# Optimization experiments

Measured on AMD Instinct MI355X. Metric: run time of the kernel, lower is better.

The kernel has to match this reference:

```python
import jax, jax.numpy as jnp
import numpy as np

H = 16         # num query heads
KV = 8         # num kv heads
HD = 64        # head_dim
WINDOW = 512   # sliding window size
ROPE_BASE = 10000.0


def rotate_half(x):
    x1, x2 = x[..., : x.shape[-1] // 2], x[..., x.shape[-1] // 2 :]
    return jnp.concatenate((-x2, x1), axis=-1)


def rope_cos_sin(seq_len, dim, dtype):
    inv_freq = 1.0 / (ROPE_BASE ** (jnp.arange(0, dim, 2, dtype=jnp.float32) / dim))
    t = jnp.arange(seq_len, dtype=jnp.float32)
    freqs = jnp.outer(t, inv_freq)              # [S, dim/2]
    emb = jnp.concatenate((freqs, freqs), axis=-1)  # [S, dim]
    return jnp.cos(emb).astype(dtype), jnp.sin(emb).astype(dtype)


def setup_inputs() -> dict:
    key = jax.random.key(0)
    ks = jax.random.split(key, 5)
    B, S, D = 2, 2048, 1024
    std = 0.02
    return {
        "hidden_states": jax.random.normal(ks[0], (B, S, D), dtype=jnp.float32),
        "Wq": jax.random.normal(ks[1], (D, H * HD), dtype=jnp.float32) * std,
        "Wk": jax.random.normal(ks[2], (D, KV * HD), dtype=jnp.float32) * std,
        "Wv": jax.random.normal(ks[3], (D, KV * HD), dtype=jnp.float32) * std,
        "Wo": jax.random.normal(ks[4], (H * HD, D), dtype=jnp.float32) * std,
    }


def reference(hidden_states, Wq, Wk, Wv, Wo):
    B, S, D = hidden_states.shape
    n_rep = H // KV

    q = (hidden_states @ Wq).reshape(B, S, H, HD).transpose(0, 2, 1, 3)   # [B,H,S,hd]
    k = (hidden_states @ Wk).reshape(B, S, KV, HD).transpose(0, 2, 1, 3)  # [B,KV,S,hd]
    v = (hidden_states @ Wv).reshape(B, S, KV, HD).transpose(0, 2, 1, 3)

    cos, sin = rope_cos_sin(S, HD, q.dtype)  # [S,hd]
    cos = cos[None, None]
    sin = sin[None, None]
    q = q * cos + rotate_half(q) * sin
    k = k * cos + rotate_half(k) * sin

    # repeat kv heads for GQA ([:, :, None] expand + reshape == repeat along head axis)
    k = jnp.repeat(k, n_rep, axis=1)  # [B,H,S,hd]
    v = jnp.repeat(v, n_rep, axis=1)

    scores = jnp.einsum("bhqd,bhkd->bhqk", q, k) / jnp.sqrt(jnp.asarray(HD, q.dtype))
    i = jnp.arange(S)[:, None]
    j = jnp.arange(S)[None, :]
    allowed = (j <= i) & (j >= i - WINDOW)  # causal + sliding window
    scores = jnp.where(allowed[None, None], scores, -jnp.inf)

    attn = jax.nn.softmax(scores, axis=-1)
    out = jnp.einsum("bhqk,bhkd->bhqd", attn, v)          # [B,H,S,hd]
    out = out.transpose(0, 2, 1, 3).reshape(B, S, H * HD)  # [B,S,D]
    return out @ Wo
```

## Files before the change

### kernel.cpp

```cpp
#include <hip/hip_runtime.h>
#include <hip/hip_bf16.h>

typedef __attribute__((ext_vector_type(8))) short short8;
typedef __attribute__((ext_vector_type(4))) float f32x4;

#define S_LEN 2048
#define NH 16
#define NKV 8
#define HD 64
#define WIN 512
#define DMODEL 1024
#define LOG2_10000 13.287712379549449f

#define GLOAD16(g, l)                                                        \
    __builtin_amdgcn_global_load_lds(                                        \
        (const __attribute__((address_space(1))) unsigned int*)(g),          \
        (__attribute__((address_space(3))) unsigned int*)(l), 16, 0, 0)

__global__ void cast_bf16_kernel(const float* __restrict__ X,
                                 __hip_bfloat16* __restrict__ Y, int n) {
    int i = (blockIdx.x * 256 + threadIdx.x) * 4;
    if (i + 3 < n) {
        float4 v = *reinterpret_cast<const float4*>(X + i);
        Y[i + 0] = __float2bfloat16(v.x);
        Y[i + 1] = __float2bfloat16(v.y);
        Y[i + 2] = __float2bfloat16(v.z);
        Y[i + 3] = __float2bfloat16(v.w);
    }
}

__global__ void transpose_cast4_kernel(const float* __restrict__ W0,
                                       const float* __restrict__ W1,
                                       const float* __restrict__ W2,
                                       const float* __restrict__ W3,
                                       __hip_bfloat16* __restrict__ WqkvT,
                                       __hip_bfloat16* __restrict__ WoT) {
    __shared__ float tile[32][33];
    const int K = DMODEL;
    const float* W;
    __hip_bfloat16* WT;
    int N;
    switch (blockIdx.z) {
        case 0: W = W0; WT = WqkvT;                          N = 1024; break;
        case 1: W = W1; WT = WqkvT + (size_t)1024 * K;       N = 512;  break;
        case 2: W = W2; WT = WqkvT + (size_t)1536 * K;       N = 512;  break;
        default: W = W3; WT = WoT;                           N = 1024; break;
    }
    if ((int)blockIdx.x * 32 >= N) return;
    int nx = blockIdx.x * 32 + threadIdx.x;
    int k0 = blockIdx.y * 32;
#pragma unroll
    for (int r = 0; r < 4; ++r) {
        int k = k0 + threadIdx.y + r * 8;
        tile[threadIdx.y + r * 8][threadIdx.x] = W[(size_t)k * N + nx];
    }
    __syncthreads();
#pragma unroll
    for (int r = 0; r < 4; ++r) {
        int nn = blockIdx.x * 32 + threadIdx.y + r * 8;
        int kk = k0 + threadIdx.x;
        WT[(size_t)nn * K + kk] = __float2bfloat16(tile[threadIdx.x][threadIdx.y + r * 8]);
    }
}

template <int MODE>
__global__ __launch_bounds__(128) void gemm128_kernel(
    const __hip_bfloat16* __restrict__ A,
    const __hip_bfloat16* __restrict__ BT,
    void* __restrict__ o0, void* __restrict__ o1, void* __restrict__ o2,
    int N, int K) {
    __shared__ __hip_bfloat16 ldsA[2][128 * 32];
    __shared__ __hip_bfloat16 ldsB[2][64 * 32];
    const int tx = threadIdx.x;
    const int wave = tx >> 6;
    const int lane = tx & 63;
    const int l16 = lane & 15;
    const int quad = lane >> 4;
    const int col0 = blockIdx.x * 64;
    const int row0 = blockIdx.y * 128;
    const int wrow = wave * 64;

    f32x4 acc[4][4] = {};

    const int arow = tx >> 2;
    const int kc8 = (tx & 3) * 8;
    const __hip_bfloat16* gA = A + (size_t)(row0 + arow) * K + kc8;
    const __hip_bfloat16* gB = BT + (size_t)(col0 + arow) * K + kc8;

    auto stage = [&](int k0, int bf) {
        char* lA = (char*)(&ldsA[bf][0]) + tx * 16;
        char* lB = (char*)(&ldsB[bf][0]) + tx * 16;
#pragma unroll
        for (int r = 0; r < 4; ++r)
            GLOAD16(gA + (size_t)(r * 32) * K + k0, lA + r * 2048);
#pragma unroll
        for (int r = 0; r < 2; ++r)
            GLOAD16(gB + (size_t)(r * 32) * K + k0, lB + r * 2048);
    };

    stage(0, 0);
    int buf = 0;
    for (int k0 = 0; k0 < K; k0 += 32) {
        __syncthreads();
        if (k0 + 32 < K) stage(k0 + 32, buf ^ 1);
        short8 af[4], bf4[4];
#pragma unroll
        for (int i = 0; i < 4; ++i) {
            af[i] = *reinterpret_cast<const short8*>(
                &ldsA[buf][0] + (wrow + i * 16 + l16) * 32 + quad * 8);
            bf4[i] = *reinterpret_cast<const short8*>(
                &ldsB[buf][0] + (i * 16 + l16) * 32 + quad * 8);
        }
#pragma unroll
        for (int mi = 0; mi < 4; ++mi)
#pragma unroll
            for (int ni = 0; ni < 4; ++ni)
                acc[mi][ni] = __builtin_amdgcn_mfma_f32_16x16x32_bf16(
                    af[mi], bf4[ni], acc[mi][ni], 0, 0, 0);
        buf ^= 1;
    }

    const int rbase = row0 + wrow;
    if (MODE == 0) {
        const int cbaseg = col0;
        const bool isQ = (cbaseg < DMODEL);
        const bool isK = (cbaseg >= DMODEL) && (cbaseg < DMODEL + 512);
        if (isQ || isK) {
            float invf[2];
            invf[0] = exp2f(-(float)(l16)      * (LOG2_10000 / 32.0f));
            invf[1] = exp2f(-(float)(16 + l16) * (LOG2_10000 / 32.0f));
#pragma unroll
            for (int mi = 0; mi < 4; ++mi)
#pragma unroll
                for (int r = 0; r < 4; ++r) {
                    int srow = (rbase + mi * 16 + quad * 4 + r) & (S_LEN - 1);
#pragma unroll
                    for (int ni = 0; ni < 2; ++ni) {
                        float ang = (float)srow * invf[ni];
                        float c = __cosf(ang), s = __sinf(ang);
                        float x1 = acc[mi][ni][r], x2 = acc[mi][ni + 2][r];
                        acc[mi][ni][r]     = x1 * c - x2 * s;
                        acc[mi][ni + 2][r] = x2 * c + x1 * s;
                    }
                }
            __hip_bfloat16* Co = (__hip_bfloat16*)(isQ ? o0 : o1);
            int cbase = isQ ? cbaseg : cbaseg - DMODEL;
            int rowstride = isQ ? (NH * HD) : (NKV * HD);
#pragma unroll
            for (int mi = 0; mi < 4; ++mi)
#pragma unroll
                for (int ni = 0; ni < 4; ++ni) {
                    size_t col = cbase + ni * 16 + l16;
#pragma unroll
                    for (int r = 0; r < 4; ++r)
                        Co[(size_t)(rbase + mi * 16 + quad * 4 + r) * rowstride + col] =
                            __float2bfloat16(acc[mi][ni][r]);
                }
        } else {
            __hip_bfloat16* VTo = (__hip_bfloat16*)o2;
            int bb = row0 >> 11;
#pragma unroll
            for (int mi = 0; mi < 4; ++mi) {
                int s = ((rbase + mi * 16 + quad * 4) & (S_LEN - 1));
#pragma unroll
                for (int ni = 0; ni < 4; ++ni) {
                    int colv = cbaseg - 1536 + ni * 16 + l16;
                    int vh = colv >> 6, d = colv & 63;
                    alignas(8) __hip_bfloat16 hv[4];
#pragma unroll
                    for (int r = 0; r < 4; ++r) hv[r] = __float2bfloat16(acc[mi][ni][r]);
                    *reinterpret_cast<ushort4*>(
                        VTo + ((size_t)(bb * NKV + vh) * HD + d) * S_LEN + s) =
                        *reinterpret_cast<ushort4*>(hv);
                }
            }
        }
    } else {
        float* Co = (float*)o0;
#pragma unroll
        for (int mi = 0; mi < 4; ++mi)
#pragma unroll
            for (int ni = 0; ni < 4; ++ni) {
                size_t col = col0 + ni * 16 + l16;
#pragma unroll
                for (int r = 0; r < 4; ++r)
                    Co[(size_t)(rbase + mi * 16 + quad * 4 + r) * N + col] = acc[mi][ni][r];
            }
    }
}

__global__ __launch_bounds__(256, 3) void attn_mfma_kernel(
    const __hip_bfloat16* __restrict__ Q,
    const __hip_bfloat16* __restrict__ K,
    const __hip_bfloat16* __restrict__ VT,
    __hip_bfloat16* __restrict__ O) {
    __shared__ __hip_bfloat16 ldsK[2][64][64];
    __shared__ __hip_bfloat16 ldsVT[2][64][64];
    __shared__ __hip_bfloat16 ldsP[4][2][16][80];
    const int tx = threadIdx.x;
    const int wave = tx >> 6;
    const int lane = tx & 63;
    const int l16 = lane & 15;
    const int quad = lane >> 4;
    const int q0 = blockIdx.x * 64;
    const int kvh = blockIdx.y;
    const int b = blockIdx.z;
    const int qi = q0 + wave * 16 + l16;

    short8 aq[2][2];
#pragma unroll
    for (int hh = 0; hh < 2; ++hh) {
        const __hip_bfloat16* qp =
            Q + (size_t)(b * S_LEN + qi) * (NH * HD) + (2 * kvh + hh) * HD + quad * 8;
        aq[hh][0] = *reinterpret_cast<const short8*>(qp);
        aq[hh][1] = *reinterpret_cast<const short8*>(qp + 32);
    }
    f32x4 acc_o[2][4] = {};
    float m[2] = {-1e30f, -1e30f}, l[2] = {0.f, 0.f};
    const float SL2 = 0.125f * 1.4426950408889634f;

    const int s_row = tx >> 3;
    const int s_c8 = (((tx & 7) ^ (s_row & 7))) * 8;
    const int sw = (l16 & 7);
    auto stage = [&](int j0, int bf) {
        char* lk = (char*)(&ldsK[bf][0][0]) + tx * 16;
        char* lv = (char*)(&ldsVT[bf][0][0]) + tx * 16;
#pragma unroll
        for (int r = 0; r < 2; ++r) {
            int row = s_row + r * 32;
            GLOAD16(K + (size_t)(b * S_LEN + j0 + row) * (NKV * HD) + kvh * HD + s_c8,
                    lk + r * 4096);
            GLOAD16(VT + ((size_t)(b * NKV + kvh) * HD + row) * S_LEN + j0 + s_c8,
                    lv + r * 4096);
        }
    };

    const int kstart = (q0 >= WIN) ? (q0 - WIN) : 0;
    stage(kstart, 0);
    int buf = 0;

    for (int j0 = kstart; j0 <= q0; j0 += 64) {
        __syncthreads();
        if (j0 + 64 <= q0) stage(j0 + 64, buf ^ 1);

        f32x4 sacc[2][4] = {};
#pragma unroll
        for (int t = 0; t < 4; ++t) {
            const __hip_bfloat16* krow = &ldsK[buf][t * 16 + l16][0];
            short8 bk0 = *reinterpret_cast<const short8*>(krow + ((quad ^ sw) * 8));
            short8 bk1 = *reinterpret_cast<const short8*>(krow + (((4 + quad) ^ sw) * 8));
            sacc[0][t] = __builtin_amdgcn_mfma_f32_16x16x32_bf16(bk0, aq[0][0], sacc[0][t], 0, 0, 0);
            sacc[0][t] = __builtin_amdgcn_mfma_f32_16x16x32_bf16(bk1, aq[0][1], sacc[0][t], 0, 0, 0);
            sacc[1][t] = __builtin_amdgcn_mfma_f32_16x16x32_bf16(bk0, aq[1][0], sacc[1][t], 0, 0, 0);
            sacc[1][t] = __builtin_amdgcn_mfma_f32_16x16x32_bf16(bk1, aq[1][1], sacc[1][t], 0, 0, 0);
        }

        const bool need_mask = (j0 == q0) || (q0 >= WIN && j0 == kstart);
#pragma unroll
        for (int hh = 0; hh < 2; ++hh) {
            float sv[4][4];
            if (need_mask) {
#pragma unroll
                for (int t = 0; t < 4; ++t)
#pragma unroll
                    for (int r = 0; r < 4; ++r) {
                        int j = j0 + t * 16 + quad * 4 + r;
                        bool ok = (j <= qi) && (j + WIN >= qi);
                        sv[t][r] = ok ? sacc[hh][t][r] * SL2 : -1e30f;
                    }
            } else {
#pragma unroll
                for (int t = 0; t < 4; ++t)
#pragma unroll
                    for (int r = 0; r < 4; ++r) sv[t][r] = sacc[hh][t][r] * SL2;
            }
            float cm = -1e30f;
#pragma unroll
            for (int t = 0; t < 4; ++t)
#pragma unroll
                for (int r = 0; r < 4; ++r) cm = fmaxf(cm, sv[t][r]);
            cm = fmaxf(cm, __shfl_xor(cm, 16));
            cm = fmaxf(cm, __shfl_xor(cm, 32));
            float mn = fmaxf(m[hh], cm);
            float alpha = exp2f(m[hh] - mn);
            m[hh] = mn;
            float sp = 0.f;
#pragma unroll
            for (int t = 0; t < 4; ++t)
#pragma unroll
                for (int r = 0; r < 4; ++r) { sv[t][r] = exp2f(sv[t][r] - mn); sp += sv[t][r]; }
            sp += __shfl_xor(sp, 16);
            sp += __shfl_xor(sp, 32);
            l[hh] = l[hh] * alpha + sp;
#pragma unroll
            for (int t = 0; t < 4; ++t)
#pragma unroll
                for (int r = 0; r < 4; ++r) acc_o[hh][t][r] *= alpha;
#pragma unroll
            for (int t = 0; t < 4; ++t) {
                alignas(8) __hip_bfloat16 hp[4];
#pragma unroll
                for (int r = 0; r < 4; ++r) hp[r] = __float2bfloat16(sv[t][r]);
                *reinterpret_cast<ushort4*>(&ldsP[wave][hh][l16][t * 16 + quad * 4]) =
                    *reinterpret_cast<ushort4*>(hp);
            }
        }

#pragma unroll
        for (int ks = 0; ks < 2; ++ks) {
            short8 pf0 = *reinterpret_cast<const short8*>(
                &ldsP[wave][0][l16][ks * 32 + quad * 8]);
            short8 pf1 = *reinterpret_cast<const short8*>(
                &ldsP[wave][1][l16][ks * 32 + quad * 8]);
#pragma unroll
            for (int t = 0; t < 4; ++t) {
                const __hip_bfloat16* vrow = &ldsVT[buf][t * 16 + l16][0];
                short8 vf = *reinterpret_cast<const short8*>(
                    vrow + (((ks * 4 + quad) ^ sw) * 8));
                acc_o[0][t] = __builtin_amdgcn_mfma_f32_16x16x32_bf16(vf, pf0, acc_o[0][t], 0, 0, 0);
                acc_o[1][t] = __builtin_amdgcn_mfma_f32_16x16x32_bf16(vf, pf1, acc_o[1][t], 0, 0, 0);
            }
        }
        buf ^= 1;
    }

#pragma unroll
    for (int hh = 0; hh < 2; ++hh) {
        float inv = 1.f / l[hh];
        __hip_bfloat16* op =
            O + (size_t)(b * S_LEN + qi) * (NH * HD) + (2 * kvh + hh) * HD;
#pragma unroll
        for (int t = 0; t < 4; ++t) {
            alignas(8) __hip_bfloat16 ho[4];
#pragma unroll
            for (int r = 0; r < 4; ++r) ho[r] = __float2bfloat16(acc_o[hh][t][r] * inv);
            *reinterpret_cast<ushort4*>(op + t * 16 + quad * 4) =
                *reinterpret_cast<ushort4*>(ho);
        }
    }
}

extern "C" void kernel_launch(void* const* d_in, const int* in_sizes, int n_in,
                              void* d_out, int out_size, void* d_ws, size_t ws_size,
                              hipStream_t stream) {
    const float* X  = (const float*)d_in[0];
    const float* Wq = (const float*)d_in[1];
    const float* Wk = (const float*)d_in[2];
    const float* Wv = (const float*)d_in[3];
    const float* Wo = (const float*)d_in[4];
    float* out = (float*)d_out;

    const int ROWS = 2 * S_LEN;
    char* ws = (char*)d_ws;
    size_t off = 0;
    __hip_bfloat16* Xb     = (__hip_bfloat16*)(ws + off); off += (size_t)ROWS * DMODEL * 2;
    __hip_bfloat16* WqkvT  = (__hip_bfloat16*)(ws + off); off += (size_t)2048 * DMODEL * 2;
    __hip_bfloat16* WoT    = (__hip_bfloat16*)(ws + off); off += (size_t)DMODEL * DMODEL * 2;
    __hip_bfloat16* Qb     = (__hip_bfloat16*)(ws + off); off += (size_t)ROWS * (NH * HD) * 2;
    __hip_bfloat16* Kb     = (__hip_bfloat16*)(ws + off); off += (size_t)ROWS * (NKV * HD) * 2;
    __hip_bfloat16* VTg    = (__hip_bfloat16*)(ws + off); off += (size_t)ROWS * (NKV * HD) * 2;
    __hip_bfloat16* Ob     = (__hip_bfloat16*)(ws + off); off += (size_t)ROWS * (NH * HD) * 2;

    cast_bf16_kernel<<<(ROWS * DMODEL) / (256 * 4), 256, 0, stream>>>(X, Xb, ROWS * DMODEL);
    transpose_cast4_kernel<<<dim3(32, 32, 4), dim3(32, 8), 0, stream>>>(
        Wq, Wk, Wv, Wo, WqkvT, WoT);

    gemm128_kernel<0><<<dim3(2048 / 64, ROWS / 128), 128, 0, stream>>>(
        Xb, WqkvT, Qb, Kb, VTg, 2048, DMODEL);

    attn_mfma_kernel<<<dim3(S_LEN / 64, NKV, 2), 256, 0, stream>>>(Qb, Kb, VTg, Ob);

    gemm128_kernel<1><<<dim3(DMODEL / 64, ROWS / 128), 128, 0, stream>>>(
        Ob, WoT, out, nullptr, nullptr, DMODEL, DMODEL);
}
```

Baseline: 166.4 us.

## Split attention grid per query head instead of per KV head pair

The attention kernel now launches one block per query head rather than one per KV head handling both grouped query heads. This doubles the grid to 1024 blocks and halves per-thread register state, and launch bounds are raised to 4 blocks per CU. The P tile in LDS shrinks to one head and uses an XOR-swizzled layout in place of padding to avoid bank conflicts. In exchange, each K/V tile is now loaded twice from global memory, once for each head sharing it.

```diff
diff --git a/kernel.cpp b/kernel.cpp
--- a/kernel.cpp
+++ b/kernel.cpp
@@ -189,34 +189,34 @@
     }
 }
 
-__global__ __launch_bounds__(256, 3) void attn_mfma_kernel(
+__global__ __launch_bounds__(256, 4) void attn_mfma_kernel(
     const __hip_bfloat16* __restrict__ Q,
     const __hip_bfloat16* __restrict__ K,
     const __hip_bfloat16* __restrict__ VT,
     __hip_bfloat16* __restrict__ O) {
     __shared__ __hip_bfloat16 ldsK[2][64][64];
     __shared__ __hip_bfloat16 ldsVT[2][64][64];
-    __shared__ __hip_bfloat16 ldsP[4][2][16][80];
+    __shared__ __hip_bfloat16 ldsP[4][16][64];
     const int tx = threadIdx.x;
     const int wave = tx >> 6;
     const int lane = tx & 63;
     const int l16 = lane & 15;
     const int quad = lane >> 4;
     const int q0 = blockIdx.x * 64;
-    const int kvh = blockIdx.y;
+    const int h = blockIdx.y;
+    const int kvh = h >> 1;
     const int b = blockIdx.z;
     const int qi = q0 + wave * 16 + l16;
 
-    short8 aq[2][2];
-#pragma unroll
-    for (int hh = 0; hh < 2; ++hh) {
+    short8 aq[2];
+    {
         const __hip_bfloat16* qp =
-            Q + (size_t)(b * S_LEN + qi) * (NH * HD) + (2 * kvh + hh) * HD + quad * 8;
-        aq[hh][0] = *reinterpret_cast<const short8*>(qp);
-        aq[hh][1] = *reinterpret_cast<const short8*>(qp + 32);
-    }
-    f32x4 acc_o[2][4] = {};
-    float m[2] = {-1e30f, -1e30f}, l[2] = {0.f, 0.f};
+            Q + (size_t)(b * S_LEN + qi) * (NH * HD) + h * HD + quad * 8;
+        aq[0] = *reinterpret_cast<const short8*>(qp);
+        aq[1] = *reinterpret_cast<const short8*>(qp + 32);
+    }
+    f32x4 acc_o[4] = {};
+    float m = -1e30f, l = 0.f;
     const float SL2 = 0.125f * 1.4426950408889634f;
 
     const int s_row = tx >> 3;
@@ -239,101 +239,94 @@
     stage(kstart, 0);
     int buf = 0;
 
+    char* prow = (char*)(&ldsP[wave][l16][0]);
+
     for (int j0 = kstart; j0 <= q0; j0 += 64) {
         __syncthreads();
         if (j0 + 64 <= q0) stage(j0 + 64, buf ^ 1);
 
-        f32x4 sacc[2][4] = {};
+        f32x4 sacc[4] = {};
 #pragma unroll
         for (int t = 0; t < 4; ++t) {
             const __hip_bfloat16* krow = &ldsK[buf][t * 16 + l16][0];
             short8 bk0 = *reinterpret_cast<const short8*>(krow + ((quad ^ sw) * 8));
             short8 bk1 = *reinterpret_cast<const short8*>(krow + (((4 + quad) ^ sw) * 8));
-            sacc[0][t] = __builtin_amdgcn_mfma_f32_16x16x32_bf16(bk0, aq[0][0], sacc[0][t], 0, 0, 0);
-            sacc[0][t] = __builtin_amdgcn_mfma_f32_16x16x32_bf16(bk1, aq[0][1], sacc[0][t], 0, 0, 0);
-            sacc[1][t] = __builtin_amdgcn_mfma_f32_16x16x32_bf16(bk0, aq[1][0], sacc[1][t], 0, 0, 0);
-            sacc[1][t] = __builtin_amdgcn_mfma_f32_16x16x32_bf16(bk1, aq[1][1], sacc[1][t], 0, 0, 0);
+            sacc[t] = __builtin_amdgcn_mfma_f32_16x16x32_bf16(bk0, aq[0], sacc[t], 0, 0, 0);
+            sacc[t] = __builtin_amdgcn_mfma_f32_16x16x32_bf16(bk1, aq[1], sacc[t], 0, 0, 0);
         }
 
         const bool need_mask = (j0 == q0) || (q0 >= WIN && j0 == kstart);
-#pragma unroll
-        for (int hh = 0; hh < 2; ++hh) {
-            float sv[4][4];
-            if (need_mask) {
-#pragma unroll
-                for (int t = 0; t < 4; ++t)
-#pragma unroll
-                    for (int r = 0; r < 4; ++r) {
-                        int j = j0 + t * 16 + quad * 4 + r;
-                        bool ok = (j <= qi) && (j + WIN >= qi);
-                        sv[t][r] = ok ? sacc[hh][t][r] * SL2 : -1e30f;
-                    }
-            } else {
-#pragma unroll
-                for (int t = 0; t < 4; ++t)
-#pragma unroll
-                    for (int r = 0; r < 4; ++r) sv[t][r] = sacc[hh][t][r] * SL2;
-            }
-            float cm = -1e30f;
+        float sv[4][4];
+        if (need_mask) {
 #pragma unroll
             for (int t = 0; t < 4; ++t)
 #pragma unroll
-                for (int r = 0; r < 4; ++r) cm = fmaxf(cm, sv[t][r]);
-            cm = fmaxf(cm, __shfl_xor(cm, 16));
-            cm = fmaxf(cm, __shfl_xor(cm, 32));
-            float mn = fmaxf(m[hh], cm);
-            float alpha = exp2f(m[hh] - mn);
-            m[hh] = mn;
-            float sp = 0.f;
+                for (int r = 0; r < 4; ++r) {
+                    int j = j0 + t * 16 + quad * 4 + r;
+                    bool ok = (j <= qi) && (j + WIN >= qi);
+                    sv[t][r] = ok ? sacc[t][r] * SL2 : -1e30f;
+                }
+        } else {
 #pragma unroll
             for (int t = 0; t < 4; ++t)
 #pragma unroll
-                for (int r = 0; r < 4; ++r) { sv[t][r] = exp2f(sv[t][r] - mn); sp += sv[t][r]; }
-            sp += __shfl_xor(sp, 16);
-            sp += __shfl_xor(sp, 32);
-            l[hh] = l[hh] * alpha + sp;
-#pragma unroll
-            for (int t = 0; t < 4; ++t)
-#pragma unroll
-                for (int r = 0; r < 4; ++r) acc_o[hh][t][r] *= alpha;
-#pragma unroll
-            for (int t = 0; t < 4; ++t) {
-                alignas(8) __hip_bfloat16 hp[4];
-#pragma unroll
-                for (int r = 0; r < 4; ++r) hp[r] = __float2bfloat16(sv[t][r]);
-                *reinterpret_cast<ushort4*>(&ldsP[wave][hh][l16][t * 16 + quad * 4]) =
-                    *reinterpret_cast<ushort4*>(hp);
-            }
+                for (int r = 0; r < 4; ++r) sv[t][r] = sacc[t][r] * SL2;
+        }
+        float cm = -1e30f;
+#pragma unroll
+        for (int t = 0; t < 4; ++t)
+#pragma unroll
+            for (int r = 0; r < 4; ++r) cm = fmaxf(cm, sv[t][r]);
+        cm = fmaxf(cm, __shfl_xor(cm, 16));
+        cm = fmaxf(cm, __shfl_xor(cm, 32));
+        float mn = fmaxf(m, cm);
+        float alpha = exp2f(m - mn);
+        m = mn;
+        float sp = 0.f;
+#pragma unroll
+        for (int t = 0; t < 4; ++t)
+#pragma unroll
+            for (int r = 0; r < 4; ++r) { sv[t][r] = exp2f(sv[t][r] - mn); sp += sv[t][r]; }
+        sp += __shfl_xor(sp, 16);
+        sp += __shfl_xor(sp, 32);
+        l = l * alpha + sp;
+#pragma unroll
+        for (int t = 0; t < 4; ++t)
+#pragma unroll
+            for (int r = 0; r < 4; ++r) acc_o[t][r] *= alpha;
+#pragma unroll
+        for (int t = 0; t < 4; ++t) {
+            alignas(8) __hip_bfloat16 hp[4];
+#pragma unroll
+            for (int r = 0; r < 4; ++r) hp[r] = __float2bfloat16(sv[t][r]);
+            int swb = ((((2 * t + (quad >> 1)) ^ (l16 & 7)) << 4) | ((quad & 1) << 3));
+            *reinterpret_cast<ushort4*>(prow + swb) = *reinterpret_cast<ushort4*>(hp);
         }
 
 #pragma unroll
         for (int ks = 0; ks < 2; ++ks) {
-            short8 pf0 = *reinterpret_cast<const short8*>(
-                &ldsP[wave][0][l16][ks * 32 + quad * 8]);
-            short8 pf1 = *reinterpret_cast<const short8*>(
-                &ldsP[wave][1][l16][ks * 32 + quad * 8]);
+            short8 pf = *reinterpret_cast<const short8*>(
+                prow + (((4 * ks + quad) ^ (l16 & 7)) << 4));
 #pragma unroll
             for (int t = 0; t < 4; ++t) {
                 const __hip_bfloat16* vrow = &ldsVT[buf][t * 16 + l16][0];
                 short8 vf = *reinterpret_cast<const short8*>(
                     vrow + (((ks * 4 + quad) ^ sw) * 8));
-                acc_o[0][t] = __builtin_amdgcn_mfma_f32_16x16x32_bf16(vf, pf0, acc_o[0][t], 0, 0, 0);
-                acc_o[1][t] = __builtin_amdgcn_mfma_f32_16x16x32_bf16(vf, pf1, acc_o[1][t], 0, 0, 0);
+                acc_o[t] = __builtin_amdgcn_mfma_f32_16x16x32_bf16(vf, pf, acc_o[t], 0, 0, 0);
             }
         }
         buf ^= 1;
     }
 
-#pragma unroll
-    for (int hh = 0; hh < 2; ++hh) {
-        float inv = 1.f / l[hh];
+    {
+        float inv = 1.f / l;
         __hip_bfloat16* op =
-            O + (size_t)(b * S_LEN + qi) * (NH * HD) + (2 * kvh + hh) * HD;
+            O + (size_t)(b * S_LEN + qi) * (NH * HD) + h * HD;
 #pragma unroll
         for (int t = 0; t < 4; ++t) {
             alignas(8) __hip_bfloat16 ho[4];
 #pragma unroll
-            for (int r = 0; r < 4; ++r) ho[r] = __float2bfloat16(acc_o[hh][t][r] * inv);
+            for (int r = 0; r < 4; ++r) ho[r] = __float2bfloat16(acc_o[t][r] * inv);
             *reinterpret_cast<ushort4*>(op + t * 16 + quad * 4) =
                 *reinterpret_cast<ushort4*>(ho);
         }
@@ -368,7 +361,7 @@
     gemm128_kernel<0><<<dim3(2048 / 64, ROWS / 128), 128, 0, stream>>>(
         Xb, WqkvT, Qb, Kb, VTg, 2048, DMODEL);
 
-    attn_mfma_kernel<<<dim3(S_LEN / 64, NKV, 2), 256, 0, stream>>>(Qb, Kb, VTg, Ob);
+    attn_mfma_kernel<<<dim3(S_LEN / 64, NH, 2), 256, 0, stream>>>(Qb, Kb, VTg, Ob);
 
     gemm128_kernel<1><<<dim3(DMODEL / 64, ROWS / 128), 128, 0, stream>>>(
         Ob, WoT, out, nullptr, nullptr, DMODEL, DMODEL);
```

Result: faster. 161.9 us (-2.7%).
